# Performance work log

Hardware: AMD Instinct MI355X
Metric: run time of the kernel (lower is better)

Reference implementation:

```python
import jax, jax.numpy as jnp
import numpy as np

RADIUS = 8
DIMS = (2, 3)


def box_filter_1d(x, dim, r):
    # cumsum along dim, then sliding-window sum via prefix-sum differences,
    # with zero padding at the edges (mirrors the torch cumsum+cat trick).
    cs = jnp.cumsum(x, axis=dim)
    cs = jnp.swapaxes(cs, dim, 0)
    head = cs[r:2 * r + 1]                       # left edge: partial windows
    mid = cs[2 * r + 1:] - cs[:-2 * r - 1]       # full windows
    tail = cs[-1:] - cs[-2 * r - 1:-r - 1]       # right edge: partial windows
    out = jnp.concatenate([head, mid, tail], axis=0)
    return jnp.swapaxes(out, dim, 0)


def setup_inputs() -> dict:
    key = jax.random.key(0)
    tensor = jax.random.normal(key, (8, 32, 512, 512), dtype=jnp.float32)
    return {"tensor": tensor}


def reference(tensor):
    out = tensor
    for dim in DIMS:  # fixed, small structural loop over filtered axes
        assert out.shape[dim] > 2 * RADIUS
        out = box_filter_1d(out, dim, RADIUS)
    return out
```

## Files before the change

### kernel.cpp

```cpp
#include <hip/hip_runtime.h>

#define RADIUS 8
#define N 512
#define TR 32
#define LSTRIDE (N + 1)
#define NXCD 8
#define NWG (8 * 32 * (N / TR))

__global__ __launch_bounds__(512, 4)
void box_kernel(const float* __restrict__ in, float* __restrict__ out) {
    __shared__ float tile[TR * LSTRIDE];

    const int bid = blockIdx.x;
    const int blk = (bid % NXCD) * (NWG / NXCD) + bid / NXCD;

    const int img   = blk >> 4;
    const int strip = blk & 15;
    const int r0    = strip * TR;
    const float* __restrict__ ibase = in  + (size_t)img * N * N;
    float* __restrict__       obase = out + (size_t)img * N * N;
    const int c = threadIdx.x;

    float x[TR + 2 * RADIUS];
#pragma unroll
    for (int k = 0; k < TR + 2 * RADIUS; ++k) {
        const int row = r0 + k - RADIUS;
        x[k] = (row >= 0 && row < N) ? ibase[(size_t)row * N + c] : 0.0f;
    }
    float vs = 0.0f;
#pragma unroll
    for (int k = 0; k <= 2 * RADIUS; ++k) vs += x[k];
#pragma unroll
    for (int i = 0; i < TR; ++i) {
        tile[i * LSTRIDE + c] = vs;
        if (i + 1 < TR) vs += x[i + 2 * RADIUS + 1] - x[i];
    }
    __syncthreads();

    const int hrow = threadIdx.x & (TR - 1);
    const int seg  = threadIdx.x >> 5;
    const int c0   = seg * 32;
    const float* trow = &tile[hrow * LSTRIDE];
    float h[32];
    float hs = 0.0f;
#pragma unroll
    for (int k = -RADIUS; k <= RADIUS; ++k) {
        const int col = c0 + k;
        if (col >= 0 && col < N) hs += trow[col];
    }
#pragma unroll
    for (int j = 0; j < 32; ++j) {
        h[j] = hs;
        const int ac = c0 + j + 1 + RADIUS;
        const int sc = c0 + j - RADIUS;
        const float a = (ac < N) ? trow[ac] : 0.0f;
        const float s = (sc >= 0) ? trow[sc] : 0.0f;
        hs += a - s;
    }
    __syncthreads();

    float* twrow = &tile[hrow * LSTRIDE];
#pragma unroll
    for (int j = 0; j < 32; ++j) twrow[c0 + j] = h[j];
    __syncthreads();

#pragma unroll
    for (int i = 0; i < TR; ++i) {
        obase[(size_t)(r0 + i) * N + c] = tile[i * LSTRIDE + c];
    }
}

extern "C" void kernel_launch(void* const* d_in, const int* in_sizes, int n_in,
                              void* d_out, int out_size, void* d_ws, size_t ws_size,
                              hipStream_t stream) {
    const float* in = (const float*)d_in[0];
    float* out = (float*)d_out;
    dim3 grid(NWG);
    dim3 block(512);
    hipLaunchKernelGGL(box_kernel, grid, block, 0, stream, in, out);
}
```

Baseline: 107.7 us.

## Process four row strips per block with rolling halo buffer and direct vector stores

Each block now handles four consecutive 32-row strips of an image, keeping a 48-row ring buffer in registers so the 16-row vertical halo is loaded once per group rather than re-read for every strip. The next strip's rows are prefetched after the first barrier so the loads can overlap the horizontal pass. The horizontal results are written straight to global memory as float4 stores from registers, removing the second shared-memory round trip and one barrier. The trade-offs are a quarter as many blocks, higher register pressure from the 48-float buffer plus 32 outputs, and store lanes that each write a 128-byte segment of a different row rather than coalescing across a single row.

```diff
diff --git a/kernel.cpp b/kernel.cpp
--- a/kernel.cpp
+++ b/kernel.cpp
@@ -3,9 +3,10 @@
 #define RADIUS 8
 #define N 512
 #define TR 32
+#define SPB 4
 #define LSTRIDE (N + 1)
 #define NXCD 8
-#define NWG (8 * 32 * (N / TR))
+#define NWG (8 * 32 * (N / (TR * SPB)))
 
 __global__ __launch_bounds__(512, 4)
 void box_kernel(const float* __restrict__ in, float* __restrict__ out) {
@@ -14,59 +15,73 @@
     const int bid = blockIdx.x;
     const int blk = (bid % NXCD) * (NWG / NXCD) + bid / NXCD;
 
-    const int img   = blk >> 4;
-    const int strip = blk & 15;
-    const int r0    = strip * TR;
+    const int img   = blk >> 2;
+    const int grp   = blk & 3;
+    const int rbase = grp * (TR * SPB);
     const float* __restrict__ ibase = in  + (size_t)img * N * N;
     float* __restrict__       obase = out + (size_t)img * N * N;
     const int c = threadIdx.x;
 
-    float x[TR + 2 * RADIUS];
+    float x[48];
 #pragma unroll
-    for (int k = 0; k < TR + 2 * RADIUS; ++k) {
-        const int row = r0 + k - RADIUS;
+    for (int k = 0; k < 48; ++k) {
+        const int row = rbase + k - RADIUS;
         x[k] = (row >= 0 && row < N) ? ibase[(size_t)row * N + c] : 0.0f;
     }
-    float vs = 0.0f;
-#pragma unroll
-    for (int k = 0; k <= 2 * RADIUS; ++k) vs += x[k];
-#pragma unroll
-    for (int i = 0; i < TR; ++i) {
-        tile[i * LSTRIDE + c] = vs;
-        if (i + 1 < TR) vs += x[i + 2 * RADIUS + 1] - x[i];
-    }
-    __syncthreads();
 
     const int hrow = threadIdx.x & (TR - 1);
     const int seg  = threadIdx.x >> 5;
     const int c0   = seg * 32;
-    const float* trow = &tile[hrow * LSTRIDE];
-    float h[32];
-    float hs = 0.0f;
-#pragma unroll
-    for (int k = -RADIUS; k <= RADIUS; ++k) {
-        const int col = c0 + k;
-        if (col >= 0 && col < N) hs += trow[col];
-    }
-#pragma unroll
-    for (int j = 0; j < 32; ++j) {
-        h[j] = hs;
-        const int ac = c0 + j + 1 + RADIUS;
-        const int sc = c0 + j - RADIUS;
-        const float a = (ac < N) ? trow[ac] : 0.0f;
-        const float s = (sc >= 0) ? trow[sc] : 0.0f;
-        hs += a - s;
-    }
-    __syncthreads();
-
-    float* twrow = &tile[hrow * LSTRIDE];
-#pragma unroll
-    for (int j = 0; j < 32; ++j) twrow[c0 + j] = h[j];
-    __syncthreads();
 
 #pragma unroll
-    for (int i = 0; i < TR; ++i) {
-        obase[(size_t)(r0 + i) * N + c] = tile[i * LSTRIDE + c];
+    for (int s = 0; s < SPB; ++s) {
+        const int b  = (32 * s) % 48;
+        const int r0 = rbase + s * TR;
+
+        float vs = 0.0f;
+#pragma unroll
+        for (int k = 0; k <= 2 * RADIUS; ++k) vs += x[(b + k) % 48];
+#pragma unroll
+        for (int i = 0; i < TR; ++i) {
+            tile[i * LSTRIDE + c] = vs;
+            if (i + 1 < TR) vs += x[(b + i + 2 * RADIUS + 1) % 48] - x[(b + i) % 48];
+        }
+        __syncthreads();
+
+        if (s + 1 < SPB) {
+#pragma unroll
+            for (int k = 0; k < 32; ++k) {
+                const int row = r0 + TR + RADIUS + k;
+                x[(b + k) % 48] = (row < N) ? ibase[(size_t)row * N + c] : 0.0f;
+            }
+        }
+
+        const float* trow = &tile[hrow * LSTRIDE];
+        float hs = 0.0f;
+#pragma unroll
+        for (int k = -RADIUS; k <= RADIUS; ++k) {
+            const int col = c0 + k;
+            if (col >= 0 && col < N) hs += trow[col];
+        }
+        float h[32];
+#pragma unroll
+        for (int j = 0; j < 32; ++j) {
+            h[j] = hs;
+            const int ac = c0 + j + 1 + RADIUS;
+            const int sc = c0 + j - RADIUS;
+            const float a  = (ac < N) ? trow[ac] : 0.0f;
+            const float sb = (sc >= 0) ? trow[sc] : 0.0f;
+            hs += a - sb;
+        }
+
+        float* orow = obase + (size_t)(r0 + hrow) * N + c0;
+#pragma unroll
+        for (int g = 0; g < 8; ++g) {
+            *reinterpret_cast<float4*>(orow + 4 * g) =
+                make_float4(h[4 * g], h[4 * g + 1], h[4 * g + 2], h[4 * g + 3]);
+        }
+
+        if (s + 1 < SPB) __syncthreads();
     }
 }
 
```

Result: slower. 155.9 us (+44.8%).
